# Kernel optimization log

Measured on AMD Instinct MI355X. Metric: run time of the kernel, lower is better.

## Reference

```python
import jax, jax.numpy as jnp
import numpy as np


def setup_inputs() -> dict:
    key = jax.random.key(0)
    k1, k2 = jax.random.split(key)
    batch, d_model, L = 4096, 1024, 2048
    # binary inputs in {0,1} as in torch.randint(0, 2, ...)
    x = jax.random.randint(k1, (batch, L), 0, 2, dtype=jnp.int32)
    references = jax.random.randint(k2, (d_model, L), 0, 2).astype(jnp.float32)
    return {"x": x, "references": references}


def reference(x, references):
    # Hamming distance between binary vectors a,b in {0,1}:
    #   sum(a != b) = sum(a) + sum(b) - 2 * a.b
    # This avoids materializing the (batch, d_model, L) broadcast tensor
    # while computing exactly the same values as the original module.
    L = x.shape[-1]
    xf = x.astype(jnp.float32)                     # (B, L)
    dot = jnp.einsum('bl,dl->bd', xf, references)  # (B, D)
    sum_x = jnp.sum(xf, axis=-1, keepdims=True)    # (B, 1)
    sum_r = jnp.sum(references, axis=-1)           # (D,)
    hamming = sum_x + sum_r[None, :] - 2.0 * dot   # (B, D)
    mean = L / 2
    std = 0.5 * (L ** 0.5)
    return (hamming - mean) / std
```

## Files before the change

### kernel.cpp

```cpp
#include <hip/hip_runtime.h>
#include <stdint.h>

constexpr int B_ROWS = 4096;
constexpr int D_ROWS = 1024;
constexpr int L_LEN  = 2048;
constexpr int LB     = L_LEN / 2;

using int32x4 = __attribute__((ext_vector_type(4))) int;
using int32x8 = __attribute__((ext_vector_type(8))) int;
using f32x16  = __attribute__((ext_vector_type(16))) float;

__global__ __launch_bounds__(256) void convert_fp4_kernel(
    const int* __restrict__ x, const float* __restrict__ r,
    uint32_t* __restrict__ xq, uint32_t* __restrict__ rq,
    int groups_x, int groups_total)
{
  const int tid = blockIdx.x * blockDim.x + threadIdx.x;
  const int nth = gridDim.x * blockDim.x;
  for (int g = tid; g < groups_total; g += nth) {
    uint32_t wo;
    if (g < groups_x) {
      const int4 v0 = *reinterpret_cast<const int4*>(x + (size_t)g * 8);
      const int4 v1 = *reinterpret_cast<const int4*>(x + (size_t)g * 8 + 4);
      wo  = (v0.x ? 0xAu : 0x2u);
      wo |= (v0.y ? 0xAu : 0x2u) << 4;
      wo |= (v0.z ? 0xAu : 0x2u) << 8;
      wo |= (v0.w ? 0xAu : 0x2u) << 12;
      wo |= (v1.x ? 0xAu : 0x2u) << 16;
      wo |= (v1.y ? 0xAu : 0x2u) << 20;
      wo |= (v1.z ? 0xAu : 0x2u) << 24;
      wo |= (v1.w ? 0xAu : 0x2u) << 28;
      xq[g] = wo;
    } else {
      const int gr = g - groups_x;
      const float4 v0 = *reinterpret_cast<const float4*>(r + (size_t)gr * 8);
      const float4 v1 = *reinterpret_cast<const float4*>(r + (size_t)gr * 8 + 4);
      wo  = (v0.x != 0.0f ? 0xAu : 0x2u);
      wo |= (v0.y != 0.0f ? 0xAu : 0x2u) << 4;
      wo |= (v0.z != 0.0f ? 0xAu : 0x2u) << 8;
      wo |= (v0.w != 0.0f ? 0xAu : 0x2u) << 12;
      wo |= (v1.x != 0.0f ? 0xAu : 0x2u) << 16;
      wo |= (v1.y != 0.0f ? 0xAu : 0x2u) << 20;
      wo |= (v1.z != 0.0f ? 0xAu : 0x2u) << 24;
      wo |= (v1.w != 0.0f ? 0xAu : 0x2u) << 28;
      rq[gr] = wo;
    }
  }
}

constexpr int BM = 128;
constexpr int BN = 64;
constexpr int BKB = 64;
constexpr int KSTEPS = LB / BKB;
constexpr int GRID_D = D_ROWS / BN;
constexpr int NWG = (B_ROWS / BM) * GRID_D;

typedef __attribute__((address_space(3))) void       as3_void;
typedef const __attribute__((address_space(1))) void as1_cvoid;

__device__ __forceinline__ void gload_lds16(const void* g, void* l) {
  __builtin_amdgcn_global_load_lds((as1_cvoid*)g, (as3_void*)l, 16, 0, 0);
}

__global__ __launch_bounds__(256) void gemm_fp4_kernel(
    const uint8_t* __restrict__ Aq, const uint8_t* __restrict__ Bq,
    float* __restrict__ out)
{
  __shared__ __align__(16) uint8_t A_lds[2][BM * BKB];
  __shared__ __align__(16) uint8_t B_lds[2][BN * BKB];

  const int lin = blockIdx.x;
  const int swz = (lin & 7) * (NWG / 8) + (lin >> 3);
  const int bm  = (swz / GRID_D) * BM;
  const int bn  = (swz % GRID_D) * BN;

  const int t    = threadIdx.x;
  const int lane = t & 63;
  const int w    = t >> 6;
  const int wr   = w >> 1;
  const int wc   = w & 1;

  const uint8_t* gA[2];
#pragma unroll
  for (int c = 0; c < 2; ++c) {
    const int r = w * 32 + c * 16 + (lane >> 2);
    gA[c] = Aq + (size_t)(bm + r) * LB + (((lane & 3) ^ ((r >> 1) & 3)) * 16);
  }
  const int rB = w * 16 + (lane >> 2);
  const uint8_t* gB0 =
      Bq + (size_t)(bn + rB) * LB + (((lane & 3) ^ ((rB >> 1) & 3)) * 16);

#define STAGE(buf, k0b) do {                                                  \
    _Pragma("unroll") for (int _c = 0; _c < 2; ++_c)                          \
      gload_lds16(gA[_c] + (k0b), A_lds[buf] + (w * 32 + _c * 16) * BKB);     \
    gload_lds16(gB0 + (k0b), B_lds[buf] + (w * 16) * BKB);                    \
  } while (0)

  f32x16 acc[2] = {};

  STAGE(0, 0);
  __syncthreads();

  for (int ks = 0; ks < KSTEPS; ++ks) {
    const int cur = ks & 1;
    if (ks + 1 < KSTEPS) STAGE(cur ^ 1, (ks + 1) * BKB);

#pragma unroll
    for (int kc = 0; kc < 2; ++kc) {
      const int rowB  = wc * 32 + (lane & 31);
      const int qB    = 2 * kc + (lane >> 5);
      const int32x4 b4 = *reinterpret_cast<const int32x4*>(
          B_lds[cur] + rowB * BKB + ((qB ^ ((rowB >> 1) & 3)) * 16));
      const int32x8 b8 = {b4[0], b4[1], b4[2], b4[3], 0, 0, 0, 0};
#pragma unroll
      for (int f = 0; f < 2; ++f) {
        const int rowA  = wr * 64 + f * 32 + (lane & 31);
        const int qA    = 2 * kc + (lane >> 5);
        const int32x4 a4 = *reinterpret_cast<const int32x4*>(
            A_lds[cur] + rowA * BKB + ((qA ^ ((rowA >> 1) & 3)) * 16));
        const int32x8 a8 = {a4[0], a4[1], a4[2], a4[3], 0, 0, 0, 0};
        acc[f] = __builtin_amdgcn_mfma_scale_f32_32x32x64_f8f6f4(
            a8, b8, acc[f], 4, 4, 0, 0x7F7F7F7F, 0, 0x7F7F7F7F);
      }
    }
    __syncthreads();
  }
#undef STAGE

  const float scale = -0.5f * 0.04419417382415922f;
  const int col = bn + wc * 32 + (lane & 31);
#pragma unroll
  for (int f = 0; f < 2; ++f) {
#pragma unroll
    for (int reg = 0; reg < 16; ++reg) {
      const int row = bm + wr * 64 + f * 32 + (reg & 3) + 8 * (reg >> 2)
                    + 4 * (lane >> 5);
      out[(size_t)row * D_ROWS + col] = acc[f][reg] * scale;
    }
  }
}

extern "C" void kernel_launch(void* const* d_in, const int* in_sizes, int n_in,
                              void* d_out, int out_size, void* d_ws, size_t ws_size,
                              hipStream_t stream) {
  const int*   x = (const int*)d_in[0];
  const float* r = (const float*)d_in[1];
  float*     out = (float*)d_out;

  uint8_t* Aq = (uint8_t*)d_ws;
  uint8_t* Bq = Aq + (size_t)B_ROWS * LB;

  const int groups_x = B_ROWS * L_LEN / 8;
  const int groups_r = D_ROWS * L_LEN / 8;
  const int groups_total = groups_x + groups_r;

  convert_fp4_kernel<<<2048, 256, 0, stream>>>(
      x, r, (uint32_t*)Aq, (uint32_t*)Bq, groups_x, groups_total);

  gemm_fp4_kernel<<<NWG, 256, 0, stream>>>(Aq, Bq, out);
}
```

Before: 27.38 us.

## Triple-buffer LDS staging in FP4 GEMM with vmcnt-based waits

Moves the GEMM main loop from double to triple LDS buffering, so the global-to-LDS loads are issued two k-steps ahead. Each step now has a single barrier, preceded by an explicit s_waitcnt vmcnt(3) that waits only for the older stage instead of draining all loads. The goal is to hide global load latency behind MFMA work and to drop the trailing __syncthreads of every iteration. In exchange, LDS use per workgroup rises by half, which can lower occupancy. The hand-written waitcnt also relies on each stage issuing exactly three loads.

```diff
diff --git a/kernel.cpp b/kernel.cpp
--- a/kernel.cpp
+++ b/kernel.cpp
@@ -66,8 +66,8 @@
     const uint8_t* __restrict__ Aq, const uint8_t* __restrict__ Bq,
     float* __restrict__ out)
 {
-  __shared__ __align__(16) uint8_t A_lds[2][BM * BKB];
-  __shared__ __align__(16) uint8_t B_lds[2][BN * BKB];
+  __shared__ __align__(16) uint8_t A_lds[3][BM * BKB];
+  __shared__ __align__(16) uint8_t B_lds[3][BN * BKB];
 
   const int lin = blockIdx.x;
   const int swz = (lin & 7) * (NWG / 8) + (lin >> 3);
@@ -96,36 +96,45 @@
     gload_lds16(gB0 + (k0b), B_lds[buf] + (w * 16) * BKB);                    \
   } while (0)
 
+#define COMPUTE(cur) do {                                                     \
+    _Pragma("unroll") for (int kc = 0; kc < 2; ++kc) {                        \
+      const int rowB = wc * 32 + (lane & 31);                                 \
+      const int qB   = 2 * kc + (lane >> 5);                                  \
+      const int32x4 b4 = *reinterpret_cast<const int32x4*>(                   \
+          B_lds[cur] + rowB * BKB + ((qB ^ ((rowB >> 1) & 3)) * 16));         \
+      const int32x8 b8 = {b4[0], b4[1], b4[2], b4[3], 0, 0, 0, 0};            \
+      _Pragma("unroll") for (int f = 0; f < 2; ++f) {                         \
+        const int rowA = wr * 64 + f * 32 + (lane & 31);                      \
+        const int qA   = 2 * kc + (lane >> 5);                                \
+        const int32x4 a4 = *reinterpret_cast<const int32x4*>(                 \
+            A_lds[cur] + rowA * BKB + ((qA ^ ((rowA >> 1) & 3)) * 16));       \
+        const int32x8 a8 = {a4[0], a4[1], a4[2], a4[3], 0, 0, 0, 0};          \
+        acc[f] = __builtin_amdgcn_mfma_scale_f32_32x32x64_f8f6f4(             \
+            a8, b8, acc[f], 4, 4, 0, 0x7F7F7F7F, 0, 0x7F7F7F7F);              \
+      }                                                                       \
+    } } while (0)
+
   f32x16 acc[2] = {};
 
   STAGE(0, 0);
-  __syncthreads();
+  STAGE(1, BKB);
 
-  for (int ks = 0; ks < KSTEPS; ++ks) {
-    const int cur = ks & 1;
-    if (ks + 1 < KSTEPS) STAGE(cur ^ 1, (ks + 1) * BKB);
+#pragma unroll 3
+  for (int ks = 0; ks < KSTEPS - 1; ++ks) {
+    const int cur = ks % 3;
+    asm volatile("s_waitcnt vmcnt(3)" ::: "memory");
+    __builtin_amdgcn_sched_barrier(0);
+    __builtin_amdgcn_s_barrier();
+    if (ks + 2 < KSTEPS) STAGE((ks + 2) % 3, (ks + 2) * BKB);
+    COMPUTE(cur);
+  }
+  asm volatile("s_waitcnt vmcnt(0)" ::: "memory");
+  __builtin_amdgcn_sched_barrier(0);
+  __builtin_amdgcn_s_barrier();
+  COMPUTE(0);
 
-#pragma unroll
-    for (int kc = 0; kc < 2; ++kc) {
-      const int rowB  = wc * 32 + (lane & 31);
-      const int qB    = 2 * kc + (lane >> 5);
-      const int32x4 b4 = *reinterpret_cast<const int32x4*>(
-          B_lds[cur] + rowB * BKB + ((qB ^ ((rowB >> 1) & 3)) * 16));
-      const int32x8 b8 = {b4[0], b4[1], b4[2], b4[3], 0, 0, 0, 0};
-#pragma unroll
-      for (int f = 0; f < 2; ++f) {
-        const int rowA  = wr * 64 + f * 32 + (lane & 31);
-        const int qA    = 2 * kc + (lane >> 5);
-        const int32x4 a4 = *reinterpret_cast<const int32x4*>(
-            A_lds[cur] + rowA * BKB + ((qA ^ ((rowA >> 1) & 3)) * 16));
-        const int32x8 a8 = {a4[0], a4[1], a4[2], a4[3], 0, 0, 0, 0};
-        acc[f] = __builtin_amdgcn_mfma_scale_f32_32x32x64_f8f6f4(
-            a8, b8, acc[f], 4, 4, 0, 0x7F7F7F7F, 0, 0x7F7F7F7F);
-      }
-    }
-    __syncthreads();
-  }
 #undef STAGE
+#undef COMPUTE
 
   const float scale = -0.5f * 0.04419417382415922f;
   const int col = bn + wc * 32 + (lane & 31);
```

After: 25.02 us. -8.6%, faster.

## Pre-pack operands into MFMA fragment layout and drop LDS staging

Applied to the files above, without the earlier changes.

The conversion kernel now writes FP4 operands directly in the per-lane MFMA fragment order, so each wave reads its A and B fragments with coalesced 16-byte global loads. The GEMM drops LDS double buffering and barriers and uses 512-thread blocks on a 256-block grid, each wave computing a 64x32 tile straight from global/L2. This removes LDS traffic and synchronisation but loses inter-wave data sharing through LDS, relies on L2 for reuse, and has no explicit prefetch pipeline to hide load latency.

```diff
diff --git a/kernel.cpp b/kernel.cpp
--- a/kernel.cpp
+++ b/kernel.cpp
@@ -4,24 +4,35 @@
 constexpr int B_ROWS = 4096;
 constexpr int D_ROWS = 1024;
 constexpr int L_LEN  = 2048;
-constexpr int LB     = L_LEN / 2;
+
+constexpr int MBLKS = B_ROWS / 32;
+constexpr int NBLKS = D_ROWS / 32;
+constexpr int KCH   = L_LEN / 64;
+
+constexpr int A_DWORDS = MBLKS * KCH * 64 * 4;
+constexpr int B_DWORDS = NBLKS * KCH * 64 * 4;
 
 using int32x4 = __attribute__((ext_vector_type(4))) int;
 using int32x8 = __attribute__((ext_vector_type(8))) int;
 using f32x16  = __attribute__((ext_vector_type(16))) float;
 
-__global__ __launch_bounds__(256) void convert_fp4_kernel(
+__global__ __launch_bounds__(256) void convert_frag_kernel(
     const int* __restrict__ x, const float* __restrict__ r,
-    uint32_t* __restrict__ xq, uint32_t* __restrict__ rq,
-    int groups_x, int groups_total)
+    uint32_t* __restrict__ Af, uint32_t* __restrict__ Bf)
 {
   const int tid = blockIdx.x * blockDim.x + threadIdx.x;
   const int nth = gridDim.x * blockDim.x;
-  for (int g = tid; g < groups_total; g += nth) {
-    uint32_t wo;
-    if (g < groups_x) {
-      const int4 v0 = *reinterpret_cast<const int4*>(x + (size_t)g * 8);
-      const int4 v1 = *reinterpret_cast<const int4*>(x + (size_t)g * 8 + 4);
+  for (int dw = tid; dw < A_DWORDS + B_DWORDS; dw += nth) {
+    if (dw < A_DWORDS) {
+      const int slot = dw >> 2, q = dw & 3;
+      const int lane = slot & 63, kc = (slot >> 6) & (KCH - 1);
+      const int mblk = slot >> 11;
+      const int row  = mblk * 32 + (lane & 31);
+      const int k0   = kc * 64 + (lane >> 5) * 32 + q * 8;
+      const int* s = x + (size_t)row * L_LEN + k0;
+      const int4 v0 = *reinterpret_cast<const int4*>(s);
+      const int4 v1 = *reinterpret_cast<const int4*>(s + 4);
+      uint32_t wo;
       wo  = (v0.x ? 0xAu : 0x2u);
       wo |= (v0.y ? 0xAu : 0x2u) << 4;
       wo |= (v0.z ? 0xAu : 0x2u) << 8;
@@ -30,11 +41,18 @@
       wo |= (v1.y ? 0xAu : 0x2u) << 20;
       wo |= (v1.z ? 0xAu : 0x2u) << 24;
       wo |= (v1.w ? 0xAu : 0x2u) << 28;
-      xq[g] = wo;
+      Af[dw] = wo;
     } else {
-      const int gr = g - groups_x;
-      const float4 v0 = *reinterpret_cast<const float4*>(r + (size_t)gr * 8);
-      const float4 v1 = *reinterpret_cast<const float4*>(r + (size_t)gr * 8 + 4);
+      const int dwb  = dw - A_DWORDS;
+      const int slot = dwb >> 2, q = dwb & 3;
+      const int lane = slot & 63, kc = (slot >> 6) & (KCH - 1);
+      const int nblk = slot >> 11;
+      const int row  = nblk * 32 + (lane & 31);
+      const int k0   = kc * 64 + (lane >> 5) * 32 + q * 8;
+      const float* s = r + (size_t)row * L_LEN + k0;
+      const float4 v0 = *reinterpret_cast<const float4*>(s);
+      const float4 v1 = *reinterpret_cast<const float4*>(s + 4);
+      uint32_t wo;
       wo  = (v0.x != 0.0f ? 0xAu : 0x2u);
       wo |= (v0.y != 0.0f ? 0xAu : 0x2u) << 4;
       wo |= (v0.z != 0.0f ? 0xAu : 0x2u) << 8;
@@ -43,100 +61,58 @@
       wo |= (v1.y != 0.0f ? 0xAu : 0x2u) << 20;
       wo |= (v1.z != 0.0f ? 0xAu : 0x2u) << 24;
       wo |= (v1.w != 0.0f ? 0xAu : 0x2u) << 28;
-      rq[gr] = wo;
+      Bf[dwb] = wo;
     }
   }
 }
 
-constexpr int BM = 128;
-constexpr int BN = 64;
-constexpr int BKB = 64;
-constexpr int KSTEPS = LB / BKB;
-constexpr int GRID_D = D_ROWS / BN;
-constexpr int NWG = (B_ROWS / BM) * GRID_D;
+constexpr int NWG = 256;
 
-typedef __attribute__((address_space(3))) void       as3_void;
-typedef const __attribute__((address_space(1))) void as1_cvoid;
-
-__device__ __forceinline__ void gload_lds16(const void* g, void* l) {
-  __builtin_amdgcn_global_load_lds((as1_cvoid*)g, (as3_void*)l, 16, 0, 0);
-}
-
-__global__ __launch_bounds__(256) void gemm_fp4_kernel(
-    const uint8_t* __restrict__ Aq, const uint8_t* __restrict__ Bq,
+__global__ __launch_bounds__(512, 2) void gemm_fp4_kernel(
+    const int32x4* __restrict__ Af, const int32x4* __restrict__ Bf,
     float* __restrict__ out)
 {
-  __shared__ __align__(16) uint8_t A_lds[2][BM * BKB];
-  __shared__ __align__(16) uint8_t B_lds[2][BN * BKB];
-
   const int lin = blockIdx.x;
   const int swz = (lin & 7) * (NWG / 8) + (lin >> 3);
-  const int bm  = (swz / GRID_D) * BM;
-  const int bn  = (swz % GRID_D) * BN;
+  const int mtile = swz >> 4;
+  const int ntile = swz & 15;
 
   const int t    = threadIdx.x;
   const int lane = t & 63;
   const int w    = t >> 6;
-  const int wr   = w >> 1;
-  const int wc   = w & 1;
+  const int wm   = w >> 1;
+  const int wn   = w & 1;
 
-  const uint8_t* gA[2];
-#pragma unroll
-  for (int c = 0; c < 2; ++c) {
-    const int r = w * 32 + c * 16 + (lane >> 2);
-    gA[c] = Aq + (size_t)(bm + r) * LB + (((lane & 3) ^ ((r >> 1) & 3)) * 16);
+  const int mblk0 = mtile * 8 + wm * 2;
+  const int nblk  = ntile * 2 + wn;
+
+  const int32x4* pA0 = Af + (size_t)(mblk0    ) * KCH * 64 + lane;
+  const int32x4* pA1 = Af + (size_t)(mblk0 + 1) * KCH * 64 + lane;
+  const int32x4* pB  = Bf + (size_t) nblk       * KCH * 64 + lane;
+
+  f32x16 acc0 = {}, acc1 = {};
+
+#pragma unroll 4
+  for (int kc = 0; kc < KCH; ++kc) {
+    const int32x4 b4 = pB [kc * 64];
+    const int32x4 a0 = pA0[kc * 64];
+    const int32x4 a1 = pA1[kc * 64];
+    const int32x8 b8  = {b4[0], b4[1], b4[2], b4[3], 0, 0, 0, 0};
+    const int32x8 a80 = {a0[0], a0[1], a0[2], a0[3], 0, 0, 0, 0};
+    const int32x8 a81 = {a1[0], a1[1], a1[2], a1[3], 0, 0, 0, 0};
+    acc0 = __builtin_amdgcn_mfma_scale_f32_32x32x64_f8f6f4(
+        a80, b8, acc0, 4, 4, 0, 0x7F7F7F7F, 0, 0x7F7F7F7F);
+    acc1 = __builtin_amdgcn_mfma_scale_f32_32x32x64_f8f6f4(
+        a81, b8, acc1, 4, 4, 0, 0x7F7F7F7F, 0, 0x7F7F7F7F);
   }
-  const int rB = w * 16 + (lane >> 2);
-  const uint8_t* gB0 =
-      Bq + (size_t)(bn + rB) * LB + (((lane & 3) ^ ((rB >> 1) & 3)) * 16);
-
-#define STAGE(buf, k0b) do {                                                  \
-    _Pragma("unroll") for (int _c = 0; _c < 2; ++_c)                          \
-      gload_lds16(gA[_c] + (k0b), A_lds[buf] + (w * 32 + _c * 16) * BKB);     \
-    gload_lds16(gB0 + (k0b), B_lds[buf] + (w * 16) * BKB);                    \
-  } while (0)
-
-  f32x16 acc[2] = {};
-
-  STAGE(0, 0);
-  __syncthreads();
-
-  for (int ks = 0; ks < KSTEPS; ++ks) {
-    const int cur = ks & 1;
-    if (ks + 1 < KSTEPS) STAGE(cur ^ 1, (ks + 1) * BKB);
-
-#pragma unroll
-    for (int kc = 0; kc < 2; ++kc) {
-      const int rowB  = wc * 32 + (lane & 31);
-      const int qB    = 2 * kc + (lane >> 5);
-      const int32x4 b4 = *reinterpret_cast<const int32x4*>(
-          B_lds[cur] + rowB * BKB + ((qB ^ ((rowB >> 1) & 3)) * 16));
-      const int32x8 b8 = {b4[0], b4[1], b4[2], b4[3], 0, 0, 0, 0};
-#pragma unroll
-      for (int f = 0; f < 2; ++f) {
-        const int rowA  = wr * 64 + f * 32 + (lane & 31);
-        const int qA    = 2 * kc + (lane >> 5);
-        const int32x4 a4 = *reinterpret_cast<const int32x4*>(
-            A_lds[cur] + rowA * BKB + ((qA ^ ((rowA >> 1) & 3)) * 16));
-        const int32x8 a8 = {a4[0], a4[1], a4[2], a4[3], 0, 0, 0, 0};
-        acc[f] = __builtin_amdgcn_mfma_scale_f32_32x32x64_f8f6f4(
-            a8, b8, acc[f], 4, 4, 0, 0x7F7F7F7F, 0, 0x7F7F7F7F);
-      }
-    }
-    __syncthreads();
-  }
-#undef STAGE
 
   const float scale = -0.5f * 0.04419417382415922f;
-  const int col = bn + wc * 32 + (lane & 31);
+  const int col = nblk * 32 + (lane & 31);
 #pragma unroll
-  for (int f = 0; f < 2; ++f) {
-#pragma unroll
-    for (int reg = 0; reg < 16; ++reg) {
-      const int row = bm + wr * 64 + f * 32 + (reg & 3) + 8 * (reg >> 2)
-                    + 4 * (lane >> 5);
-      out[(size_t)row * D_ROWS + col] = acc[f][reg] * scale;
-    }
+  for (int reg = 0; reg < 16; ++reg) {
+    const int rin = (reg & 3) + 8 * (reg >> 2) + 4 * (lane >> 5);
+    out[(size_t)(mblk0 * 32 + rin)       * D_ROWS + col] = acc0[reg] * scale;
+    out[(size_t)((mblk0 + 1) * 32 + rin) * D_ROWS + col] = acc1[reg] * scale;
   }
 }
 
@@ -147,15 +123,11 @@
   const float* r = (const float*)d_in[1];
   float*     out = (float*)d_out;
 
-  uint8_t* Aq = (uint8_t*)d_ws;
-  uint8_t* Bq = Aq + (size_t)B_ROWS * LB;
+  uint32_t* Af = (uint32_t*)d_ws;
+  uint32_t* Bf = Af + A_DWORDS;
 
-  const int groups_x = B_ROWS * L_LEN / 8;
-  const int groups_r = D_ROWS * L_LEN / 8;
-  const int groups_total = groups_x + groups_r;
+  convert_frag_kernel<<<2048, 256, 0, stream>>>(x, r, Af, Bf);
 
-  convert_fp4_kernel<<<2048, 256, 0, stream>>>(
-      x, r, (uint32_t*)Aq, (uint32_t*)Bq, groups_x, groups_total);
-
-  gemm_fp4_kernel<<<NWG, 256, 0, stream>>>(Aq, Bq, out);
+  gemm_fp4_kernel<<<NWG, 512, 0, stream>>>(
+      (const int32x4*)Af, (const int32x4*)Bf, out);
 }
```

Result: slower. 33.05 us (+20.7%).
